# Performance work log

Measured on AMD Instinct MI355X. Metric: run time of the kernel, lower is better.

Reference implementation:

```python
import jax, jax.numpy as jnp
import numpy as np

N_STEPS = 3  # fixed propagation depth standing in for the BFS-guided delta_st recursion


def setup_inputs() -> dict:
    key = jax.random.key(0)
    ks = jax.random.split(key, 12)
    n, d, E = 32, 96, 256
    f32 = jnp.float32
    rn = lambda k, s, sc: jax.random.normal(k, s, f32) * sc
    return {
        "node_embeddings": rn(ks[0], (n, d), 1.0),
        "edges": jax.random.randint(ks[1], (E, 2), 0, n, jnp.int32),
        "w1": rn(ks[2], (4, 4, 3), 0.3), "b1": jnp.full((4,), 0.01, f32),
        "w2": rn(ks[3], (4, 4, 3), 0.3), "b2": jnp.full((4,), 0.01, f32),
        "w3": rn(ks[4], (4, 4, 3), 0.3), "b3": jnp.full((4,), 0.01, f32),
        "fc1_w": rn(ks[5], (16, 128), 0.2), "fc1_b": jnp.full((128,), 0.01, f32),
        "fc2_w": rn(ks[6], (128, 256), 0.1), "fc2_b": jnp.full((256,), 0.01, f32),
        "fc3_w": rn(ks[7], (256, 128), 0.1), "fc3_b": jnp.full((128,), 0.01, f32),
        "fc4_w": rn(ks[8], (128, 1), 0.1), "fc4_b": jnp.full((1,), 0.01, f32),
    }


def _conv1d(x, w, b, stride):
    # x: [B, C, L], w: [O, I, K]
    y = jax.lax.conv_general_dilated(x, w, (stride,), 'VALID',
                                     dimension_numbers=('NCH', 'OIH', 'NCH'))
    return y + b[None, :, None]


def _maxpool2(x):
    return jax.lax.reduce_window(x, -jnp.inf, jax.lax.max, (1, 1, 2), (1, 1, 2), 'VALID')


def _conv_pool_stack(x, w1, b1, w2, b2, w3, b3,
                     fc1_w, fc1_b, fc2_w, fc2_b, fc3_w, fc3_b, fc4_w, fc4_b):
    # x: [B, 4, 96] -> [B]
    h = _maxpool2(jax.nn.relu(_conv1d(x, w1, b1, 2)))   # [B,4,23]
    h = _maxpool2(jax.nn.relu(_conv1d(h, w2, b2, 1)))   # [B,4,10]
    h = _maxpool2(jax.nn.relu(_conv1d(h, w3, b3, 1)))   # [B,4,4]
    h = h.reshape(h.shape[0], -1)                       # [B,16]
    h = jax.nn.relu(h @ fc1_w + fc1_b)
    h = jax.nn.relu(h @ fc2_w + fc2_b)
    h = jax.nn.relu(h @ fc3_w + fc3_b)
    return (h @ fc4_w + fc4_b)[:, 0]


def reference(node_embeddings, edges, w1, b1, w2, b2, w3, b3,
              fc1_w, fc1_b, fc2_w, fc2_b, fc3_w, fc3_b, fc4_w, fc4_b):
    n, d = node_embeddings.shape
    E = edges.shape[0]
    u_idx, v_idx = edges[:, 0], edges[:, 1]

    # All (s, t) node pairs, flattened: P = n*n (s == t masked out below).
    s_idx, t_idx = jnp.meshgrid(jnp.arange(n), jnp.arange(n), indexing='ij')
    s_idx, t_idx = s_idx.reshape(-1), t_idx.reshape(-1)
    P = n * n

    se = node_embeddings[s_idx]  # [P, d]
    te = node_embeddings[t_idx]  # [P, d]
    ue = node_embeddings[u_idx]  # [E, d]
    ve = node_embeddings[v_idx]  # [E, d]

    # stuv input: [P, E, 4, d] -> [P*E, 4, d]
    stuv = jnp.stack([
        jnp.broadcast_to(se[:, None, :], (P, E, d)),
        jnp.broadcast_to(te[:, None, :], (P, E, d)),
        jnp.broadcast_to(ue[None, :, :], (P, E, d)),
        jnp.broadcast_to(ve[None, :, :], (P, E, d)),
    ], axis=2).reshape(P * E, 4, d)

    preds = _conv_pool_stack(stuv, w1, b1, w2, b2, w3, b3,
                             fc1_w, fc1_b, fc2_w, fc2_b,
                             fc3_w, fc3_b, fc4_w, fc4_b).reshape(P, E)

    # zero out s == t pairs (the original skips them)
    preds = preds * (s_idx != t_idx).astype(preds.dtype)[:, None]

    # delta_st: propagate unit mass from s through the per-pair sparse routing
    # matrix R[u, v] = preds[p, e] for N_STEPS hops, accumulating arrivals.
    x = jax.nn.one_hot(s_idx, n, dtype=preds.dtype)  # [P, n]
    rbc = jnp.zeros((n,), preds.dtype)
    for _ in range(N_STEPS):
        gathered = x[:, u_idx] * preds                      # [P, E]
        x = jnp.zeros((P, n), preds.dtype).at[:, v_idx].add(gathered)
        rbc = rbc + x.sum(axis=0)

    return rbc / jnp.sum(rbc)
```

## Files before the change

kernel.cpp:

```cpp
#include <hip/hip_runtime.h>

constexpr int G_OFF = 0;
constexpr int H_OFF = 196608;
constexpr int PREDS_OFF = H_OFF + 49152;
constexpr int RBCP_OFF = PREDS_OFF + 262144;
constexpr int CNT_OFF = RBCP_OFF + 2048;
constexpr int W1P_OFF = CNT_OFF + 16;
constexpr int W2P_OFF = W1P_OFF + 2048;
constexpr int W3P_OFF = W2P_OFF + 16384;

typedef __attribute__((ext_vector_type(8))) short short8;
typedef __attribute__((ext_vector_type(4))) short short4v;
typedef __attribute__((ext_vector_type(4))) float f32x4;
typedef __attribute__((ext_vector_type(2))) unsigned int uint2v;

__device__ __forceinline__ unsigned short f2bf(float x) {
    unsigned u = __float_as_uint(x);
    u += 0x7FFF + ((u >> 16) & 1);
    return (unsigned short)(u >> 16);
}

__device__ __forceinline__ unsigned cvt_pk_bf16(float a, float b) {
    unsigned r;
    asm("v_cvt_pk_bf16_f32 %0, %1, %2" : "=v"(r) : "v"(a), "v"(b));
    return r;
}

template <int CTRL>
__device__ __forceinline__ float qp(float x) {
    return __int_as_float(__builtin_amdgcn_update_dpp(
        0, __float_as_int(x), CTRL, 0xF, 0xF, true));
}

__global__ void prep_all(const float* __restrict__ emb, const int* __restrict__ edges,
                         const float* __restrict__ w1, const float* __restrict__ b1,
                         const float* __restrict__ fc1_w, const float* __restrict__ fc2_w,
                         const float* __restrict__ fc3_w,
                         float* __restrict__ G, float* __restrict__ H,
                         unsigned short* __restrict__ W1p,
                         unsigned short* __restrict__ W2p, unsigned short* __restrict__ W3p,
                         float* __restrict__ rbcp_zero) {
    int b = blockIdx.x;
    if (b < 768) {
        int idx = b * 256 + threadIdx.x;
        int i = idx % 48;
        int o = (idx / 48) & 3;
        int p = idx / 192;
        int s = p >> 5, t = p & 31;
        float acc = 0.f;
        if (i < 46) {
#pragma unroll
            for (int k = 0; k < 3; k++)
                acc += w1[(o * 4 + 0) * 3 + k] * emb[s * 96 + 2 * i + k] +
                       w1[(o * 4 + 1) * 3 + k] * emb[t * 96 + 2 * i + k];
        }
        G[idx] = acc;
        return;
    }
    if (b < 960) {
        int idx = (b - 768) * 256 + threadIdx.x;
        int i = idx % 48;
        int o = (idx / 48) & 3;
        int e = idx / 192;
        int u = edges[2 * e], v = edges[2 * e + 1];
        float acc = 0.f;
        if (i < 46) {
            acc = b1[o];
#pragma unroll
            for (int k = 0; k < 3; k++)
                acc += w1[(o * 4 + 2) * 3 + k] * emb[u * 96 + 2 * i + k] +
                       w1[(o * 4 + 3) * 3 + k] * emb[v * 96 + 2 * i + k];
        }
        H[idx] = acc;
        return;
    }
    if (b < 976) {
        int t = (b - 960) * 256 + threadIdx.x;
        int j = t & 7, lane = (t >> 3) & 63, mt = t >> 9;
        int k = (lane >> 4) * 8 + j, n = mt * 16 + (lane & 15);
        float w = (k < 16) ? fc1_w[k * 128 + n] : 0.f;
        W1p[t] = f2bf(w);
        return;
    }
    if (b < 1104) {
        int t = (b - 976) * 256 + threadIdx.x;
        int j = t & 7, lane = (t >> 3) & 63, ks = (t >> 9) & 3, mt = t >> 11;
        int k = ks * 32 + (lane >> 4) * 8 + j, n = mt * 16 + (lane & 15);
        W2p[t] = f2bf(fc2_w[k * 256 + n]);
        return;
    }
    if (b < 1232) {
        int t = (b - 1104) * 256 + threadIdx.x;
        int j = t & 7, lane = (t >> 3) & 63, ks = (t >> 9) & 7, mt = t >> 12;
        int k = ks * 32 + (lane >> 4) * 8 + j, n = mt * 16 + (lane & 15);
        W3p[t] = f2bf(fc3_w[k * 128 + n]);
        return;
    }
    for (int k = threadIdx.x; k < 2064; k += 256) rbcp_zero[k] = 0.f;
}

__global__ __launch_bounds__(256, 4)
void mlp_kernel(const float* __restrict__ G, const float* __restrict__ H,
                const float* __restrict__ w2, const float* __restrict__ b2,
                const float* __restrict__ w3, const float* __restrict__ b3,
                const float* __restrict__ fc1_b, const float* __restrict__ fc2_b,
                const float* __restrict__ fc3_b,
                const float* __restrict__ fc4_w, const float* __restrict__ fc4_b,
                const unsigned short* __restrict__ W1p, const unsigned short* __restrict__ W2p,
                const unsigned short* __restrict__ W3p,
                float* __restrict__ preds) {
    __shared__ __align__(16) float smem[8448];
    unsigned short* X1 = (unsigned short*)smem;
    unsigned short* X3f = (unsigned short*)smem;
    unsigned short* X2 = (unsigned short*)(smem + 4096);
    float* part = smem + 8192;

    const int tid = threadIdx.x;
    const int bid = (blockIdx.x & 7) * 512 + (blockIdx.x >> 3);
    const int p = bid >> 2;
    const int e0 = (bid & 3) * 64;
    const int s = p >> 5, t = p & 31;
    if (s == t) return;

    const int lane = tid & 63, wave = tid >> 6;
    const int mrow = lane & 15, quad = lane >> 4;

    const int gsample = tid >> 2, o = tid & 3;
    float h1[23];
    {
        const int e = e0 + gsample;
        const f32x4* Gp = (const f32x4*)(G + (p * 4 + o) * 48);
        const f32x4* Hp = (const f32x4*)(H + (e * 4 + o) * 48);
        float pre[46];
#pragma unroll
        for (int q = 0; q < 12; q++) {
            f32x4 x = Gp[q] + Hp[q];
#pragma unroll
            for (int z = 0; z < 4; z++) {
                int i = 4 * q + z;
                if (i < 46) pre[i] = x[z];
            }
        }
#pragma unroll
        for (int j = 0; j < 23; j++) h1[j] = fmaxf(fmaxf(pre[2 * j], pre[2 * j + 1]), 0.f);
    }
    float h2[10];
    {
        float wm[4][3];
#pragma unroll
        for (int m = 0; m < 4; m++)
#pragma unroll
            for (int k = 0; k < 3; k++) wm[m][k] = w2[o * 12 + (o ^ m) * 3 + k];
        const float bb = b2[o];
        float win[4][3];
#pragma unroll
        for (int j = 0; j < 2; j++) {
            float x = h1[j];
            win[0][j] = x;
            win[1][j] = qp<0xB1>(x);
            win[2][j] = qp<0x4E>(x);
            win[3][j] = qp<0x1B>(x);
        }
        float pre[20];
#pragma unroll
        for (int i = 0; i < 20; i++) {
            float x = h1[i + 2];
            win[0][(i + 2) % 3] = x;
            win[1][(i + 2) % 3] = qp<0xB1>(x);
            win[2][(i + 2) % 3] = qp<0x4E>(x);
            win[3][(i + 2) % 3] = qp<0x1B>(x);
            float acc = bb;
#pragma unroll
            for (int m = 0; m < 4; m++)
#pragma unroll
                for (int k = 0; k < 3; k++)
                    acc = fmaf(wm[m][k], win[m][(i + k) % 3], acc);
            pre[i] = acc;
        }
#pragma unroll
        for (int j = 0; j < 10; j++) h2[j] = fmaxf(fmaxf(pre[2 * j], pre[2 * j + 1]), 0.f);
    }
    {
        float wm[4][3];
#pragma unroll
        for (int m = 0; m < 4; m++)
#pragma unroll
            for (int k = 0; k < 3; k++) wm[m][k] = w3[o * 12 + (o ^ m) * 3 + k];
        const float bb = b3[o];
        float win[4][3];
#pragma unroll
        for (int j = 0; j < 2; j++) {
            float x = h2[j];
            win[0][j] = x;
            win[1][j] = qp<0xB1>(x);
            win[2][j] = qp<0x4E>(x);
            win[3][j] = qp<0x1B>(x);
        }
        float pre[8];
#pragma unroll
        for (int i = 0; i < 8; i++) {
            float x = h2[i + 2];
            win[0][(i + 2) % 3] = x;
            win[1][(i + 2) % 3] = qp<0xB1>(x);
            win[2][(i + 2) % 3] = qp<0x4E>(x);
            win[3][(i + 2) % 3] = qp<0x1B>(x);
            float acc = bb;
#pragma unroll
            for (int m = 0; m < 4; m++)
#pragma unroll
                for (int k = 0; k < 3; k++)
                    acc = fmaf(wm[m][k], win[m][(i + k) % 3], acc);
            pre[i] = acc;
        }
        float v0 = fmaxf(fmaxf(pre[0], pre[1]), 0.f);
        float v1 = fmaxf(fmaxf(pre[2], pre[3]), 0.f);
        float v2 = fmaxf(fmaxf(pre[4], pre[5]), 0.f);
        float v3 = fmaxf(fmaxf(pre[6], pre[7]), 0.f);
        uint2v d;
        d.x = cvt_pk_bf16(v0, v1);
        d.y = cvt_pk_bf16(v2, v3);
        *(uint2v*)(X1 + (((o >> 1) * 64 + gsample) * 8) + (o & 1) * 4) = d;
        uint2v z2 = (uint2v){0u, 0u};
        *(uint2v*)(X1 + ((((o >> 1) + 2) * 64 + gsample) * 8) + (o & 1) * 4) = z2;
    }
    const short8* W1v = (const short8*)W1p;
    short8 w1f[2];
#pragma unroll
    for (int mtl = 0; mtl < 2; mtl++)
        w1f[mtl] = W1v[(wave * 2 + mtl) * 64 + lane];
    __syncthreads();
    {
        short8 bnt[4];
#pragma unroll
        for (int nt = 0; nt < 4; nt++)
            bnt[nt] = *(const short8*)(X1 + (quad * 64 + nt * 16 + mrow) * 8);
        f32x4 acc1[2][4];
#pragma unroll
        for (int a = 0; a < 2; a++)
#pragma unroll
            for (int b = 0; b < 4; b++) acc1[a][b] = (f32x4){0.f, 0.f, 0.f, 0.f};
#pragma unroll
        for (int mtl = 0; mtl < 2; mtl++) {
#pragma unroll
            for (int nt = 0; nt < 4; nt++)
                acc1[mtl][nt] = __builtin_amdgcn_mfma_f32_16x16x32_bf16(w1f[mtl], bnt[nt], acc1[mtl][nt], 0, 0, 0);
        }
#pragma unroll
        for (int mtl = 0; mtl < 2; mtl++) {
            const int mt = wave * 2 + mtl;
            const int n0 = mt * 16 + quad * 4;
            f32x4 b4 = *(const f32x4*)(fc1_b + n0);
#pragma unroll
            for (int nt = 0; nt < 4; nt++) {
                float x0 = fmaxf(acc1[mtl][nt][0] + b4[0], 0.f);
                float x1 = fmaxf(acc1[mtl][nt][1] + b4[1], 0.f);
                float x2 = fmaxf(acc1[mtl][nt][2] + b4[2], 0.f);
                float x3 = fmaxf(acc1[mtl][nt][3] + b4[3], 0.f);
                uint2v d;
                d.x = cvt_pk_bf16(x0, x1);
                d.y = cvt_pk_bf16(x2, x3);
                *(uint2v*)(X2 + ((n0 >> 3) * 64 + nt * 16 + mrow) * 8 + (n0 & 7)) = d;
            }
        }
    }
    __syncthreads();
    const short8* W2v = (const short8*)W2p;
    const short8* W3v = (const short8*)W3p;
    f32x4 acc2[4][4];
#pragma unroll
    for (int a = 0; a < 4; a++)
#pragma unroll
        for (int b = 0; b < 4; b++) acc2[a][b] = (f32x4){0.f, 0.f, 0.f, 0.f};
#pragma unroll
    for (int ks = 0; ks < 4; ks++) {
        short8 bfr[4];
#pragma unroll
        for (int nt = 0; nt < 4; nt++)
            bfr[nt] = *(const short8*)(X2 + ((ks * 4 + quad) * 64 + nt * 16 + mrow) * 8);
#pragma unroll
        for (int q = 0; q < 4; q++) {
            const int mt = q * 4 + wave;
            short8 ah = W2v[(mt * 4 + ks) * 64 + lane];
#pragma unroll
            for (int nt = 0; nt < 4; nt++)
                acc2[q][nt] = __builtin_amdgcn_mfma_f32_16x16x32_bf16(ah, bfr[nt], acc2[q][nt], 0, 0, 0);
        }
    }
    __syncthreads();
#pragma unroll
    for (int q = 0; q < 4; q++) {
        const int mt = q * 4 + wave;
        const int n0 = mt * 16 + quad * 4;
        f32x4 b4 = *(const f32x4*)(fc2_b + n0);
#pragma unroll
        for (int nt = 0; nt < 4; nt++) {
            float x0 = fmaxf(acc2[q][nt][0] + b4[0], 0.f);
            float x1 = fmaxf(acc2[q][nt][1] + b4[1], 0.f);
            float x2 = fmaxf(acc2[q][nt][2] + b4[2], 0.f);
            float x3 = fmaxf(acc2[q][nt][3] + b4[3], 0.f);
            uint2v d;
            d.x = cvt_pk_bf16(x0, x1);
            d.y = cvt_pk_bf16(x2, x3);
            *(uint2v*)(X3f + ((n0 >> 3) * 64 + nt * 16 + mrow) * 8 + (n0 & 7)) = d;
        }
    }
    __syncthreads();
    f32x4 acc3[2][4];
#pragma unroll
    for (int a = 0; a < 2; a++)
#pragma unroll
        for (int b = 0; b < 4; b++) acc3[a][b] = (f32x4){0.f, 0.f, 0.f, 0.f};
#pragma unroll
    for (int ks = 0; ks < 8; ks++) {
        short8 bfr[4];
#pragma unroll
        for (int nt = 0; nt < 4; nt++)
            bfr[nt] = *(const short8*)(X3f + ((ks * 4 + quad) * 64 + nt * 16 + mrow) * 8);
#pragma unroll
        for (int mtl = 0; mtl < 2; mtl++) {
            const int mt = wave * 2 + mtl;
            short8 ah = W3v[(mt * 8 + ks) * 64 + lane];
#pragma unroll
            for (int nt = 0; nt < 4; nt++)
                acc3[mtl][nt] = __builtin_amdgcn_mfma_f32_16x16x32_bf16(ah, bfr[nt], acc3[mtl][nt], 0, 0, 0);
        }
    }
    {
        float p4[4] = {0.f, 0.f, 0.f, 0.f};
#pragma unroll
        for (int mtl = 0; mtl < 2; mtl++) {
            const int mt = wave * 2 + mtl;
            const int n0 = mt * 16 + quad * 4;
            f32x4 b4 = *(const f32x4*)(fc3_b + n0);
            f32x4 w44 = *(const f32x4*)(fc4_w + n0);
#pragma unroll
            for (int nt = 0; nt < 4; nt++)
#pragma unroll
                for (int r = 0; r < 4; r++)
                    p4[nt] = fmaf(fmaxf(acc3[mtl][nt][r] + b4[r], 0.f), w44[r], p4[nt]);
        }
#pragma unroll
        for (int nt = 0; nt < 4; nt++) {
            p4[nt] += __shfl_xor(p4[nt], 16, 64);
            p4[nt] += __shfl_xor(p4[nt], 32, 64);
        }
        if (quad == 0) {
#pragma unroll
            for (int nt = 0; nt < 4; nt++)
                part[wave * 64 + nt * 16 + mrow] = p4[nt];
        }
    }
    __syncthreads();
    if (tid < 64) {
        float pred = part[tid] + part[64 + tid] + part[128 + tid] + part[192 + tid] + fc4_b[0];
        preds[p * 256 + e0 + tid] = pred;
    }
}

__global__ __launch_bounds__(256)
void prop_kernel(const int* __restrict__ edges, const float* __restrict__ preds,
                 float* __restrict__ rbc_part) {
    const int tid = threadIdx.x;
    const int wave = tid >> 6, lane = tid & 63;
    const int p = blockIdx.x * 4 + wave;
    const int s = p >> 5, t = p & 31;
    __shared__ float xw[4][32], xnw[4][32], raccw[4][32];
    int u[4], v[4];
    float pr[4];
#pragma unroll
    for (int j = 0; j < 4; j++) {
        int e = lane + 64 * j;
        u[j] = edges[2 * e];
        v[j] = edges[2 * e + 1];
        pr[j] = preds[p * 256 + e];
    }
    if (lane < 32) { xw[wave][lane] = (lane == s) ? 1.f : 0.f; raccw[wave][lane] = 0.f; }
    const bool active = (s != t);
    for (int step = 0; step < 3; step++) {
        if (lane < 32) xnw[wave][lane] = 0.f;
        __syncthreads();
        if (active) {
#pragma unroll
            for (int j = 0; j < 4; j++)
                atomicAdd(&xnw[wave][v[j]], xw[wave][u[j]] * pr[j]);
        }
        __syncthreads();
        if (lane < 32) { raccw[wave][lane] += xnw[wave][lane]; xw[wave][lane] = xnw[wave][lane]; }
        __syncthreads();
    }
    if (active && lane < 32) atomicAdd(&rbc_part[(p & 63) * 32 + lane], raccw[wave][lane]);
}

__global__ __launch_bounds__(256)
void norm_kernel(const float* __restrict__ rbc_part, float* __restrict__ out) {
    const int tid = threadIdx.x;
    const int node = tid & 31, sub = tid >> 5;
    __shared__ float red[8][32];
    float vv = 0.f;
#pragma unroll
    for (int g = 0; g < 8; g++)
        vv += rbc_part[(sub * 8 + g) * 32 + node];
    red[sub][node] = vv;
    __syncthreads();
    if (tid < 32) {
        float acc = 0.f;
#pragma unroll
        for (int sb = 0; sb < 8; sb++) acc += red[sb][tid];
        float tot = acc;
#pragma unroll
        for (int mask = 1; mask < 32; mask <<= 1) tot += __shfl_xor(tot, mask, 32);
        out[tid] = acc / tot;
    }
}

extern "C" void kernel_launch(void* const* d_in, const int* in_sizes, int n_in,
                              void* d_out, int out_size, void* d_ws, size_t ws_size,
                              hipStream_t stream) {
    const float* emb = (const float*)d_in[0];
    const int* edges = (const int*)d_in[1];
    const float* w1 = (const float*)d_in[2];
    const float* b1 = (const float*)d_in[3];
    const float* w2 = (const float*)d_in[4];
    const float* b2 = (const float*)d_in[5];
    const float* w3 = (const float*)d_in[6];
    const float* b3 = (const float*)d_in[7];
    const float* fc1_w = (const float*)d_in[8];
    const float* fc1_b = (const float*)d_in[9];
    const float* fc2_w = (const float*)d_in[10];
    const float* fc2_b = (const float*)d_in[11];
    const float* fc3_w = (const float*)d_in[12];
    const float* fc3_b = (const float*)d_in[13];
    const float* fc4_w = (const float*)d_in[14];
    const float* fc4_b = (const float*)d_in[15];

    float* ws = (float*)d_ws;
    float* G = ws + G_OFF;
    float* H = ws + H_OFF;
    float* preds = ws + PREDS_OFF;
    float* rbc_part = ws + RBCP_OFF;
    unsigned short* W1p = (unsigned short*)(ws + W1P_OFF);
    unsigned short* W2p = (unsigned short*)(ws + W2P_OFF);
    unsigned short* W3p = (unsigned short*)(ws + W3P_OFF);
    float* out = (float*)d_out;

    prep_all<<<dim3(1233), dim3(256), 0, stream>>>(emb, edges, w1, b1, fc1_w, fc2_w, fc3_w,
                                                   G, H, W1p, W2p, W3p, rbc_part);
    mlp_kernel<<<dim3(4096), dim3(256), 0, stream>>>(
        G, H, w2, b2, w3, b3, fc1_b, fc2_b, fc3_b,
        fc4_w, fc4_b, W1p, W2p, W3p, preds);
    prop_kernel<<<dim3(256), dim3(256), 0, stream>>>(edges, preds, rbc_part);
    norm_kernel<<<dim3(1), dim3(256), 0, stream>>>(rbc_part, out);
}
```

Baseline: 148.7 us.

## Split fused conv+MLP kernel into separate conv and FC kernels via workspace buffer

Splits the fused conv+MLP kernel into two. A high-occupancy conv kernel writes bf16 conv features to a new global workspace buffer, and an MFMA-based FC kernel reads them back. The aim is to stop the register-heavy scalar conv phase from limiting occupancy of the MFMA phase. The cost is an extra launch plus a global write and read of the intermediate features. The split path runs only when the workspace is large enough; otherwise it falls back to the fused kernel.

```diff
diff --git a/kernel.cpp b/kernel.cpp
--- a/kernel.cpp
+++ b/kernel.cpp
@@ -8,6 +8,9 @@
 constexpr int W1P_OFF = CNT_OFF + 16;
 constexpr int W2P_OFF = W1P_OFF + 2048;
 constexpr int W3P_OFF = W2P_OFF + 16384;
+constexpr int BASE_FLOATS = 544784;
+constexpr int C1_OFF = BASE_FLOATS;
+constexpr size_t SPLIT_WS_FLOATS = (size_t)BASE_FLOATS + 4096 * 512;
 
 typedef __attribute__((ext_vector_type(8))) short short8;
 typedef __attribute__((ext_vector_type(4))) short short4v;
@@ -99,6 +102,282 @@
     for (int k = threadIdx.x; k < 2064; k += 256) rbcp_zero[k] = 0.f;
 }
 
+__device__ __forceinline__ uint2v conv_body(
+        const float* __restrict__ G, const float* __restrict__ H,
+        const float* __restrict__ w2, const float* __restrict__ b2,
+        const float* __restrict__ w3, const float* __restrict__ b3,
+        int p, int e, int o) {
+    float h1[23];
+    {
+        const f32x4* Gp = (const f32x4*)(G + (p * 4 + o) * 48);
+        const f32x4* Hp = (const f32x4*)(H + (e * 4 + o) * 48);
+        float pre[46];
+#pragma unroll
+        for (int q = 0; q < 12; q++) {
+            f32x4 x = Gp[q] + Hp[q];
+#pragma unroll
+            for (int z = 0; z < 4; z++) {
+                int i = 4 * q + z;
+                if (i < 46) pre[i] = x[z];
+            }
+        }
+#pragma unroll
+        for (int j = 0; j < 23; j++) h1[j] = fmaxf(fmaxf(pre[2 * j], pre[2 * j + 1]), 0.f);
+    }
+    float h2[10];
+    {
+        float wm[4][3];
+#pragma unroll
+        for (int m = 0; m < 4; m++)
+#pragma unroll
+            for (int k = 0; k < 3; k++) wm[m][k] = w2[o * 12 + (o ^ m) * 3 + k];
+        const float bb = b2[o];
+        float win[4][3];
+#pragma unroll
+        for (int j = 0; j < 2; j++) {
+            float x = h1[j];
+            win[0][j] = x;
+            win[1][j] = qp<0xB1>(x);
+            win[2][j] = qp<0x4E>(x);
+            win[3][j] = qp<0x1B>(x);
+        }
+        float pre[20];
+#pragma unroll
+        for (int i = 0; i < 20; i++) {
+            float x = h1[i + 2];
+            win[0][(i + 2) % 3] = x;
+            win[1][(i + 2) % 3] = qp<0xB1>(x);
+            win[2][(i + 2) % 3] = qp<0x4E>(x);
+            win[3][(i + 2) % 3] = qp<0x1B>(x);
+            float acc = bb;
+#pragma unroll
+            for (int m = 0; m < 4; m++)
+#pragma unroll
+                for (int k = 0; k < 3; k++)
+                    acc = fmaf(wm[m][k], win[m][(i + k) % 3], acc);
+            pre[i] = acc;
+        }
+#pragma unroll
+        for (int j = 0; j < 10; j++) h2[j] = fmaxf(fmaxf(pre[2 * j], pre[2 * j + 1]), 0.f);
+    }
+    {
+        float wm[4][3];
+#pragma unroll
+        for (int m = 0; m < 4; m++)
+#pragma unroll
+            for (int k = 0; k < 3; k++) wm[m][k] = w3[o * 12 + (o ^ m) * 3 + k];
+        const float bb = b3[o];
+        float win[4][3];
+#pragma unroll
+        for (int j = 0; j < 2; j++) {
+            float x = h2[j];
+            win[0][j] = x;
+            win[1][j] = qp<0xB1>(x);
+            win[2][j] = qp<0x4E>(x);
+            win[3][j] = qp<0x1B>(x);
+        }
+        float pre[8];
+#pragma unroll
+        for (int i = 0; i < 8; i++) {
+            float x = h2[i + 2];
+            win[0][(i + 2) % 3] = x;
+            win[1][(i + 2) % 3] = qp<0xB1>(x);
+            win[2][(i + 2) % 3] = qp<0x4E>(x);
+            win[3][(i + 2) % 3] = qp<0x1B>(x);
+            float acc = bb;
+#pragma unroll
+            for (int m = 0; m < 4; m++)
+#pragma unroll
+                for (int k = 0; k < 3; k++)
+                    acc = fmaf(wm[m][k], win[m][(i + k) % 3], acc);
+            pre[i] = acc;
+        }
+        float v0 = fmaxf(fmaxf(pre[0], pre[1]), 0.f);
+        float v1 = fmaxf(fmaxf(pre[2], pre[3]), 0.f);
+        float v2 = fmaxf(fmaxf(pre[4], pre[5]), 0.f);
+        float v3 = fmaxf(fmaxf(pre[6], pre[7]), 0.f);
+        uint2v d;
+        d.x = cvt_pk_bf16(v0, v1);
+        d.y = cvt_pk_bf16(v2, v3);
+        return d;
+    }
+}
+
+__global__ __launch_bounds__(256, 8)
+void conv_kernel(const float* __restrict__ G, const float* __restrict__ H,
+                 const float* __restrict__ w2, const float* __restrict__ b2,
+                 const float* __restrict__ w3, const float* __restrict__ b3,
+                 unsigned short* __restrict__ C1) {
+    const int bid = (blockIdx.x & 7) * 512 + (blockIdx.x >> 3);
+    const int p = bid >> 2;
+    const int e0 = (bid & 3) * 64;
+    const int s = p >> 5, t = p & 31;
+    if (s == t) return;
+    const int tid = threadIdx.x;
+    const int gsample = tid >> 2, o = tid & 3;
+    uint2v d = conv_body(G, H, w2, b2, w3, b3, p, e0 + gsample, o);
+    unsigned short* C1b = C1 + (size_t)bid * 1024;
+    *(uint2v*)(C1b + (((o >> 1) * 64 + gsample) * 8) + (o & 1) * 4) = d;
+}
+
+__global__ __launch_bounds__(256, 4)
+void fc_kernel(const unsigned short* __restrict__ C1,
+               const float* __restrict__ fc1_b, const float* __restrict__ fc2_b,
+               const float* __restrict__ fc3_b,
+               const float* __restrict__ fc4_w, const float* __restrict__ fc4_b,
+               const unsigned short* __restrict__ W1p, const unsigned short* __restrict__ W2p,
+               const unsigned short* __restrict__ W3p,
+               float* __restrict__ preds) {
+    __shared__ __align__(16) float smem[8448];
+    unsigned short* X3f = (unsigned short*)smem;
+    unsigned short* X2 = (unsigned short*)(smem + 4096);
+    float* part = smem + 8192;
+
+    const int tid = threadIdx.x;
+    const int bid = (blockIdx.x & 7) * 512 + (blockIdx.x >> 3);
+    const int p = bid >> 2;
+    const int e0 = (bid & 3) * 64;
+    const int s = p >> 5, t = p & 31;
+    if (s == t) return;
+
+    const int lane = tid & 63, wave = tid >> 6;
+    const int mrow = lane & 15, quad = lane >> 4;
+
+    {
+        const short8* W1v = (const short8*)W1p;
+        short8 w1f[2];
+#pragma unroll
+        for (int mtl = 0; mtl < 2; mtl++)
+            w1f[mtl] = W1v[(wave * 2 + mtl) * 64 + lane];
+        const unsigned short* C1b = C1 + (size_t)bid * 1024;
+        const short8 z8 = (short8){0, 0, 0, 0, 0, 0, 0, 0};
+        short8 bnt[4];
+#pragma unroll
+        for (int nt = 0; nt < 4; nt++)
+            bnt[nt] = (quad < 2) ? *(const short8*)(C1b + (quad * 64 + nt * 16 + mrow) * 8) : z8;
+        f32x4 acc1[2][4];
+#pragma unroll
+        for (int a = 0; a < 2; a++)
+#pragma unroll
+            for (int b = 0; b < 4; b++) acc1[a][b] = (f32x4){0.f, 0.f, 0.f, 0.f};
+#pragma unroll
+        for (int mtl = 0; mtl < 2; mtl++) {
+#pragma unroll
+            for (int nt = 0; nt < 4; nt++)
+                acc1[mtl][nt] = __builtin_amdgcn_mfma_f32_16x16x32_bf16(w1f[mtl], bnt[nt], acc1[mtl][nt], 0, 0, 0);
+        }
+#pragma unroll
+        for (int mtl = 0; mtl < 2; mtl++) {
+            const int mt = wave * 2 + mtl;
+            const int n0 = mt * 16 + quad * 4;
+            f32x4 b4 = *(const f32x4*)(fc1_b + n0);
+#pragma unroll
+            for (int nt = 0; nt < 4; nt++) {
+                float x0 = fmaxf(acc1[mtl][nt][0] + b4[0], 0.f);
+                float x1 = fmaxf(acc1[mtl][nt][1] + b4[1], 0.f);
+                float x2 = fmaxf(acc1[mtl][nt][2] + b4[2], 0.f);
+                float x3 = fmaxf(acc1[mtl][nt][3] + b4[3], 0.f);
+                uint2v d;
+                d.x = cvt_pk_bf16(x0, x1);
+                d.y = cvt_pk_bf16(x2, x3);
+                *(uint2v*)(X2 + ((n0 >> 3) * 64 + nt * 16 + mrow) * 8 + (n0 & 7)) = d;
+            }
+        }
+    }
+    __syncthreads();
+    const short8* W2v = (const short8*)W2p;
+    const short8* W3v = (const short8*)W3p;
+    f32x4 acc2[4][4];
+#pragma unroll
+    for (int a = 0; a < 4; a++)
+#pragma unroll
+        for (int b = 0; b < 4; b++) acc2[a][b] = (f32x4){0.f, 0.f, 0.f, 0.f};
+#pragma unroll
+    for (int ks = 0; ks < 4; ks++) {
+        short8 bfr[4];
+#pragma unroll
+        for (int nt = 0; nt < 4; nt++)
+            bfr[nt] = *(const short8*)(X2 + ((ks * 4 + quad) * 64 + nt * 16 + mrow) * 8);
+#pragma unroll
+        for (int q = 0; q < 4; q++) {
+            const int mt = q * 4 + wave;
+            short8 ah = W2v[(mt * 4 + ks) * 64 + lane];
+#pragma unroll
+            for (int nt = 0; nt < 4; nt++)
+                acc2[q][nt] = __builtin_amdgcn_mfma_f32_16x16x32_bf16(ah, bfr[nt], acc2[q][nt], 0, 0, 0);
+        }
+    }
+    __syncthreads();
+#pragma unroll
+    for (int q = 0; q < 4; q++) {
+        const int mt = q * 4 + wave;
+        const int n0 = mt * 16 + quad * 4;
+        f32x4 b4 = *(const f32x4*)(fc2_b + n0);
+#pragma unroll
+        for (int nt = 0; nt < 4; nt++) {
+            float x0 = fmaxf(acc2[q][nt][0] + b4[0], 0.f);
+            float x1 = fmaxf(acc2[q][nt][1] + b4[1], 0.f);
+            float x2 = fmaxf(acc2[q][nt][2] + b4[2], 0.f);
+            float x3 = fmaxf(acc2[q][nt][3] + b4[3], 0.f);
+            uint2v d;
+            d.x = cvt_pk_bf16(x0, x1);
+            d.y = cvt_pk_bf16(x2, x3);
+            *(uint2v*)(X3f + ((n0 >> 3) * 64 + nt * 16 + mrow) * 8 + (n0 & 7)) = d;
+        }
+    }
+    __syncthreads();
+    f32x4 acc3[2][4];
+#pragma unroll
+    for (int a = 0; a < 2; a++)
+#pragma unroll
+        for (int b = 0; b < 4; b++) acc3[a][b] = (f32x4){0.f, 0.f, 0.f, 0.f};
+#pragma unroll
+    for (int ks = 0; ks < 8; ks++) {
+        short8 bfr[4];
+#pragma unroll
+        for (int nt = 0; nt < 4; nt++)
+            bfr[nt] = *(const short8*)(X3f + ((ks * 4 + quad) * 64 + nt * 16 + mrow) * 8);
+#pragma unroll
+        for (int mtl = 0; mtl < 2; mtl++) {
+            const int mt = wave * 2 + mtl;
+            short8 ah = W3v[(mt * 8 + ks) * 64 + lane];
+#pragma unroll
+            for (int nt = 0; nt < 4; nt++)
+                acc3[mtl][nt] = __builtin_amdgcn_mfma_f32_16x16x32_bf16(ah, bfr[nt], acc3[mtl][nt], 0, 0, 0);
+        }
+    }
+    {
+        float p4[4] = {0.f, 0.f, 0.f, 0.f};
+#pragma unroll
+        for (int mtl = 0; mtl < 2; mtl++) {
+            const int mt = wave * 2 + mtl;
+            const int n0 = mt * 16 + quad * 4;
+            f32x4 b4 = *(const f32x4*)(fc3_b + n0);
+            f32x4 w44 = *(const f32x4*)(fc4_w + n0);
+#pragma unroll
+            for (int nt = 0; nt < 4; nt++)
+#pragma unroll
+                for (int r = 0; r < 4; r++)
+                    p4[nt] = fmaf(fmaxf(acc3[mtl][nt][r] + b4[r], 0.f), w44[r], p4[nt]);
+        }
+#pragma unroll
+        for (int nt = 0; nt < 4; nt++) {
+            p4[nt] += __shfl_xor(p4[nt], 16, 64);
+            p4[nt] += __shfl_xor(p4[nt], 32, 64);
+        }
+        if (quad == 0) {
+#pragma unroll
+            for (int nt = 0; nt < 4; nt++)
+                part[wave * 64 + nt * 16 + mrow] = p4[nt];
+        }
+    }
+    __syncthreads();
+    if (tid < 64) {
+        float pred = part[tid] + part[64 + tid] + part[128 + tid] + part[192 + tid] + fc4_b[0];
+        preds[p * 256 + e0 + tid] = pred;
+    }
+}
+
 __global__ __launch_bounds__(256, 4)
 void mlp_kernel(const float* __restrict__ G, const float* __restrict__ H,
                 const float* __restrict__ w2, const float* __restrict__ b2,
@@ -124,101 +403,10 @@
 
     const int lane = tid & 63, wave = tid >> 6;
     const int mrow = lane & 15, quad = lane >> 4;
-
     const int gsample = tid >> 2, o = tid & 3;
-    float h1[23];
-    {
-        const int e = e0 + gsample;
-        const f32x4* Gp = (const f32x4*)(G + (p * 4 + o) * 48);
-        const f32x4* Hp = (const f32x4*)(H + (e * 4 + o) * 48);
-        float pre[46];
-#pragma unroll
-        for (int q = 0; q < 12; q++) {
-            f32x4 x = Gp[q] + Hp[q];
-#pragma unroll
-            for (int z = 0; z < 4; z++) {
-                int i = 4 * q + z;
-                if (i < 46) pre[i] = x[z];
-            }
-        }
-#pragma unroll
-        for (int j = 0; j < 23; j++) h1[j] = fmaxf(fmaxf(pre[2 * j], pre[2 * j + 1]), 0.f);
-    }
-    float h2[10];
-    {
-        float wm[4][3];
-#pragma unroll
-        for (int m = 0; m < 4; m++)
-#pragma unroll
-            for (int k = 0; k < 3; k++) wm[m][k] = w2[o * 12 + (o ^ m) * 3 + k];
-        const float bb = b2[o];
-        float win[4][3];
-#pragma unroll
-        for (int j = 0; j < 2; j++) {
-            float x = h1[j];
-            win[0][j] = x;
-            win[1][j] = qp<0xB1>(x);
-            win[2][j] = qp<0x4E>(x);
-            win[3][j] = qp<0x1B>(x);
-        }
-        float pre[20];
-#pragma unroll
-        for (int i = 0; i < 20; i++) {
-            float x = h1[i + 2];
-            win[0][(i + 2) % 3] = x;
-            win[1][(i + 2) % 3] = qp<0xB1>(x);
-            win[2][(i + 2) % 3] = qp<0x4E>(x);
-            win[3][(i + 2) % 3] = qp<0x1B>(x);
-            float acc = bb;
-#pragma unroll
-            for (int m = 0; m < 4; m++)
-#pragma unroll
-                for (int k = 0; k < 3; k++)
-                    acc = fmaf(wm[m][k], win[m][(i + k) % 3], acc);
-            pre[i] = acc;
-        }
-#pragma unroll
-        for (int j = 0; j < 10; j++) h2[j] = fmaxf(fmaxf(pre[2 * j], pre[2 * j + 1]), 0.f);
-    }
-    {
-        float wm[4][3];
-#pragma unroll
-        for (int m = 0; m < 4; m++)
-#pragma unroll
-            for (int k = 0; k < 3; k++) wm[m][k] = w3[o * 12 + (o ^ m) * 3 + k];
-        const float bb = b3[o];
-        float win[4][3];
-#pragma unroll
-        for (int j = 0; j < 2; j++) {
-            float x = h2[j];
-            win[0][j] = x;
-            win[1][j] = qp<0xB1>(x);
-            win[2][j] = qp<0x4E>(x);
-            win[3][j] = qp<0x1B>(x);
-        }
-        float pre[8];
-#pragma unroll
-        for (int i = 0; i < 8; i++) {
-            float x = h2[i + 2];
-            win[0][(i + 2) % 3] = x;
-            win[1][(i + 2) % 3] = qp<0xB1>(x);
-            win[2][(i + 2) % 3] = qp<0x4E>(x);
-            win[3][(i + 2) % 3] = qp<0x1B>(x);
-            float acc = bb;
-#pragma unroll
-            for (int m = 0; m < 4; m++)
-#pragma unroll
-                for (int k = 0; k < 3; k++)
-                    acc = fmaf(wm[m][k], win[m][(i + k) % 3], acc);
-            pre[i] = acc;
-        }
-        float v0 = fmaxf(fmaxf(pre[0], pre[1]), 0.f);
-        float v1 = fmaxf(fmaxf(pre[2], pre[3]), 0.f);
-        float v2 = fmaxf(fmaxf(pre[4], pre[5]), 0.f);
-        float v3 = fmaxf(fmaxf(pre[6], pre[7]), 0.f);
-        uint2v d;
-        d.x = cvt_pk_bf16(v0, v1);
-        d.y = cvt_pk_bf16(v2, v3);
+
+    {
+        uint2v d = conv_body(G, H, w2, b2, w3, b3, p, e0 + gsample, o);
         *(uint2v*)(X1 + (((o >> 1) * 64 + gsample) * 8) + (o & 1) * 4) = d;
         uint2v z2 = (uint2v){0u, 0u};
         *(uint2v*)(X1 + ((((o >> 1) + 2) * 64 + gsample) * 8) + (o & 1) * 4) = z2;
@@ -441,13 +629,20 @@
     unsigned short* W1p = (unsigned short*)(ws + W1P_OFF);
     unsigned short* W2p = (unsigned short*)(ws + W2P_OFF);
     unsigned short* W3p = (unsigned short*)(ws + W3P_OFF);
+    unsigned short* C1 = (unsigned short*)(ws + C1_OFF);
     float* out = (float*)d_out;
 
     prep_all<<<dim3(1233), dim3(256), 0, stream>>>(emb, edges, w1, b1, fc1_w, fc2_w, fc3_w,
                                                    G, H, W1p, W2p, W3p, rbc_part);
-    mlp_kernel<<<dim3(4096), dim3(256), 0, stream>>>(
-        G, H, w2, b2, w3, b3, fc1_b, fc2_b, fc3_b,
-        fc4_w, fc4_b, W1p, W2p, W3p, preds);
+    if (ws_size >= SPLIT_WS_FLOATS * sizeof(float)) {
+        conv_kernel<<<dim3(4096), dim3(256), 0, stream>>>(G, H, w2, b2, w3, b3, C1);
+        fc_kernel<<<dim3(4096), dim3(256), 0, stream>>>(
+            C1, fc1_b, fc2_b, fc3_b, fc4_w, fc4_b, W1p, W2p, W3p, preds);
+    } else {
+        mlp_kernel<<<dim3(4096), dim3(256), 0, stream>>>(
+            G, H, w2, b2, w3, b3, fc1_b, fc2_b, fc3_b,
+            fc4_w, fc4_b, W1p, W2p, W3p, preds);
+    }
     prop_kernel<<<dim3(256), dim3(256), 0, stream>>>(edges, preds, rbc_part);
     norm_kernel<<<dim3(1), dim3(256), 0, stream>>>(rbc_part, out);
 }
```

Result: slower. 169.6 us (+14.1%).
